# Kernel tuning notes

Measured on AMD Instinct MI355X. Metric: run time of the kernel, lower is better.

The kernel has to match this reference:

```python
import jax, jax.numpy as jnp
import numpy as np

BLOCK_SIZE = 64

def quantize_dequantize(w, block_size=BLOCK_SIZE):
    # LPBQ double quantization: block-wise abs-max -> uint4 scale1 over fp32 scale2
    out_ch, in_ch = w.shape
    pad_len = (block_size - in_ch % block_size) % block_size
    if pad_len > 0:
        w = jnp.pad(w, ((0, 0), (0, pad_len)))
    wr = w.reshape(out_ch, -1, block_size)                      # [O, nB, B]
    s1 = jnp.clip(jnp.max(jnp.abs(wr), axis=-1, keepdims=True) / 7.0, 1e-8)   # [O, nB, 1]
    s2 = jnp.clip(jnp.max(s1, axis=1, keepdims=True) / 15.0, 1e-8)            # [O, 1, 1]
    s1_q = jnp.clip(jnp.round(s1 / s2), 0.0, 15.0)
    s1_recon = s1_q * s2
    w_q = jnp.clip(jnp.round(wr / s1_recon), -8.0, 7.0)
    w_recon = (w_q * s1_recon).reshape(out_ch, -1)
    if pad_len > 0:
        w_recon = w_recon[:, :-pad_len]
    return w_recon

def setup_inputs() -> dict:
    key = jax.random.key(0)
    k1, k2, k3 = jax.random.split(key, 3)
    B, S, IN, OUT = 1, 128, 4096, 11008
    x = jax.random.normal(k1, (B, S, IN), dtype=jnp.float32)
    weight = jax.random.normal(k2, (OUT, IN), dtype=jnp.float32)
    bias = jax.random.normal(k3, (OUT,), dtype=jnp.float32)
    return {"x": x, "weight": weight, "bias": bias}

def reference(x, weight, bias):
    w_q = quantize_dequantize(weight)
    # F.linear: x @ w_q.T + bias
    return jnp.einsum('bsi,oi->bso', x, w_q) + bias
```

## Files before the change

kernel.cpp:

```cpp
#include <hip/hip_runtime.h>
#include <hip/hip_bf16.h>

#define IN_CH 4096
#define OUT_CH 11008
#define QBLK 64

#define BM 128
#define BN 64
#define BK 64
#define KCHUNKS (IN_CH / BK)
#define KSPLIT 4
#define SPLIT_CHUNKS (KCHUNKS / KSPLIT)
#define NTILES (OUT_CH / BN)
#define XCONV_BLOCKS 16
#define BPAD 72

typedef short bf16x8 __attribute__((ext_vector_type(8)));
typedef float f32x4 __attribute__((ext_vector_type(4)));

#define GLOBAL_AS __attribute__((address_space(1)))
#define LDS_AS __attribute__((address_space(3)))

__device__ inline unsigned short f2bf(float f) {
    union { __hip_bfloat16 h; unsigned short u; } cv;
    cv.h = __float2bfloat16(f);
    return cv.u;
}

__device__ inline void unpack8(unsigned v, float s1, bf16x8& o) {
#pragma unroll
    for (int i = 0; i < 4; ++i) {
        const int byte = (int)((v >> (8 * i)) & 0xFF);
        const int lo = (byte << 28) >> 28;
        const int hi = (byte << 24) >> 28;
        o[2 * i]     = (short)f2bf((float)lo * s1);
        o[2 * i + 1] = (short)f2bf((float)hi * s1);
    }
}

__global__ __launch_bounds__(256) void quant_kernel(
        const float* __restrict__ w, const float* __restrict__ x,
        signed char* __restrict__ wq, float* __restrict__ s1rT,
        unsigned short* __restrict__ xq) {
    const int tid = threadIdx.x;

    if (blockIdx.x >= OUT_CH) {
        const int bx = blockIdx.x - OUT_CH;
        for (int it = 0; it < 16; ++it) {
            const int G = it * 4096 + bx * 256 + tid;
            const int row = G >> 9;
            const int gi = G & 511;
            const int kc = gi >> 3;
            const int gp = gi & 7;
            const int gl = gp ^ (row & 7);
            const float4* src =
                (const float4*)(x + (size_t)row * IN_CH + kc * 64 + gl * 8);
            float4 a = src[0], b = src[1];
            ushort4 o0, o1;
            o0.x = f2bf(a.x); o0.y = f2bf(a.y); o0.z = f2bf(a.z); o0.w = f2bf(a.w);
            o1.x = f2bf(b.x); o1.y = f2bf(b.y); o1.z = f2bf(b.z); o1.w = f2bf(b.w);
            ushort4* dst = (ushort4*)(xq + (size_t)row * IN_CH + gi * 8);
            dst[0] = o0;
            dst[1] = o1;
        }
        return;
    }

    const int row = blockIdx.x;
    const float* wrow = w + (size_t)row * IN_CH;
    signed char* orow = wq + (size_t)row * (IN_CH / 2);

    __shared__ float s1_lds[64];

    float4 v[4];
    const int lane16 = tid & 15;

    for (int p = 0; p < 4; ++p) {
        v[p] = ((const float4*)wrow)[p * 256 + tid];
        float m = fmaxf(fmaxf(fabsf(v[p].x), fabsf(v[p].y)),
                        fmaxf(fabsf(v[p].z), fabsf(v[p].w)));
        m = fmaxf(m, __shfl_xor(m, 1));
        m = fmaxf(m, __shfl_xor(m, 2));
        m = fmaxf(m, __shfl_xor(m, 4));
        m = fmaxf(m, __shfl_xor(m, 8));
        if (lane16 == 0)
            s1_lds[p * 16 + (tid >> 4)] = fmaxf(m * (1.0f / 7.0f), 1e-8f);
    }
    __syncthreads();

    if (tid < 64) {
        float s1 = s1_lds[tid];
        float m = s1;
        m = fmaxf(m, __shfl_xor(m, 1));
        m = fmaxf(m, __shfl_xor(m, 2));
        m = fmaxf(m, __shfl_xor(m, 4));
        m = fmaxf(m, __shfl_xor(m, 8));
        m = fmaxf(m, __shfl_xor(m, 16));
        m = fmaxf(m, __shfl_xor(m, 32));
        const float s2 = fmaxf(m * (1.0f / 15.0f), 1e-8f);
        const float s1q = fminf(fmaxf(rintf(s1 / s2), 0.0f), 15.0f);
        const float s1r = s1q * s2;
        s1_lds[tid] = s1r;
        s1rT[(size_t)tid * OUT_CH + row] = s1r;
    }
    __syncthreads();

    for (int p = 0; p < 4; ++p) {
        const float s1r = s1_lds[p * 16 + (tid >> 4)];
        const int q0 = (int)fminf(fmaxf(rintf(v[p].x / s1r), -8.0f), 7.0f);
        const int q1 = (int)fminf(fmaxf(rintf(v[p].y / s1r), -8.0f), 7.0f);
        const int q2 = (int)fminf(fmaxf(rintf(v[p].z / s1r), -8.0f), 7.0f);
        const int q3 = (int)fminf(fmaxf(rintf(v[p].w / s1r), -8.0f), 7.0f);
        char2 o;
        o.x = (signed char)((q0 & 0xF) | ((q1 & 0xF) << 4));
        o.y = (signed char)((q2 & 0xF) | ((q3 & 0xF) << 4));
        ((char2*)orow)[p * 256 + tid] = o;
    }
}

__global__ __launch_bounds__(256) void gemm_kernel(
        const unsigned short* __restrict__ A, const signed char* __restrict__ WQ4,
        const float* __restrict__ s1rT, float* __restrict__ part) {
    __shared__ __align__(16) unsigned short ldsA[2][BM * BK];
    __shared__ __align__(16) unsigned short ldsB[2][BN * BPAD];

    const int tid = threadIdx.x;
    const int w = tid >> 6;
    const int l = tid & 63;
    const int wm = w >> 1;
    const int wn = w & 1;
    const int n0 = blockIdx.x * BN;
    const int kc0 = blockIdx.y * SPLIT_CHUNKS;

    const int r8 = l >> 3;
    const int sg = l & 7;

    const int brow = tid >> 2;
    const int bcg = tid & 3;

    const int lane15 = l & 15;
    const int quad = l >> 4;

    f32x4 acc[4][2] = {};

    const size_t bqBase = (size_t)(n0 + brow) * (IN_CH / 2) + bcg * 8;

    {
        const int k0 = kc0 * BK;
        for (int i = 0; i < 4; ++i) {
            const unsigned short* gp =
                A + (size_t)(i * 32 + w * 8 + r8) * IN_CH + k0 + sg * 8;
            LDS_AS unsigned short* lp =
                (LDS_AS unsigned short*)&ldsA[0][(i * 32 + w * 8) * BK];
            __builtin_amdgcn_global_load_lds((const GLOBAL_AS void*)gp,
                                             (LDS_AS void*)lp, 16, 0, 0);
        }
        const float s1 = s1rT[(size_t)kc0 * OUT_CH + n0 + brow];
        const uint2 bq = *(const uint2*)(WQ4 + bqBase + (size_t)kc0 * 32);
        bf16x8 o0, o1;
        unpack8(bq.x, s1, o0);
        unpack8(bq.y, s1, o1);
        *(bf16x8*)&ldsB[0][brow * BPAD + bcg * 16] = o0;
        *(bf16x8*)&ldsB[0][brow * BPAD + bcg * 16 + 8] = o1;
        asm volatile("s_waitcnt vmcnt(0)" ::: "memory");
        __syncthreads();
    }

    for (int t = 0; t < SPLIT_CHUNKS; ++t) {
        const int cur = t & 1;
        const int nxt = cur ^ 1;
        const bool has_next = (t + 1 < SPLIT_CHUNKS);

        uint2 bqn;
        float s1n;
        if (has_next) {
            const int kcn = kc0 + t + 1;
            const int k0n = kcn * BK;
            for (int i = 0; i < 4; ++i) {
                const unsigned short* gp =
                    A + (size_t)(i * 32 + w * 8 + r8) * IN_CH + k0n + sg * 8;
                LDS_AS unsigned short* lp =
                    (LDS_AS unsigned short*)&ldsA[nxt][(i * 32 + w * 8) * BK];
                __builtin_amdgcn_global_load_lds((const GLOBAL_AS void*)gp,
                                                 (LDS_AS void*)lp, 16, 0, 0);
            }
            s1n = s1rT[(size_t)kcn * OUT_CH + n0 + brow];
            bqn = *(const uint2*)(WQ4 + bqBase + (size_t)kcn * 32);
        }

        for (int kk = 0; kk < 2; ++kk) {
            bf16x8 af[4], bfv[2];
            const int ko = kk * 32 + quad * 8;
            for (int i = 0; i < 4; ++i) {
                const int row = wm * 64 + i * 16 + lane15;
                const int pg = ((kk * 4 + quad) ^ (row & 7)) * 8;
                af[i] = *(const bf16x8*)&ldsA[cur][row * BK + pg];
            }
            for (int j = 0; j < 2; ++j)
                bfv[j] = *(const bf16x8*)&ldsB[cur][(wn * 32 + j * 16 + lane15) * BPAD + ko];
            for (int i = 0; i < 4; ++i)
                for (int j = 0; j < 2; ++j)
                    acc[i][j] = __builtin_amdgcn_mfma_f32_16x16x32_bf16(
                        af[i], bfv[j], acc[i][j], 0, 0, 0);
        }

        if (has_next) {
            bf16x8 o0, o1;
            unpack8(bqn.x, s1n, o0);
            unpack8(bqn.y, s1n, o1);
            *(bf16x8*)&ldsB[nxt][brow * BPAD + bcg * 16] = o0;
            *(bf16x8*)&ldsB[nxt][brow * BPAD + bcg * 16 + 8] = o1;
            asm volatile("s_waitcnt vmcnt(0)" ::: "memory");
        }
        __syncthreads();
    }

    float* pbase = part + (size_t)blockIdx.y * BM * OUT_CH;
    const int m_base = wm * 64 + quad * 4;
    const int n_base = n0 + wn * 32 + lane15;
    for (int j = 0; j < 2; ++j) {
        for (int i = 0; i < 4; ++i) {
            const int m = m_base + i * 16;
            float* cp = pbase + (size_t)m * OUT_CH + n_base + j * 16;
            cp[0 * OUT_CH] = acc[i][j][0];
            cp[1 * OUT_CH] = acc[i][j][1];
            cp[2 * OUT_CH] = acc[i][j][2];
            cp[3 * OUT_CH] = acc[i][j][3];
        }
    }
}

__global__ __launch_bounds__(256) void reduce_kernel(
        const float* __restrict__ part, const float* __restrict__ bias,
        float* __restrict__ out) {
    const int m = blockIdx.y;
    const int x4 = blockIdx.x * 256 + threadIdx.x;
    if (x4 >= OUT_CH / 4) return;
    const size_t off = (size_t)m * OUT_CH + x4 * 4;

    float4 acc = ((const float4*)bias)[x4];
    for (int s = 0; s < KSPLIT; ++s) {
        float4 p = *(const float4*)(part + (size_t)s * BM * OUT_CH + off);
        acc.x += p.x; acc.y += p.y; acc.z += p.z; acc.w += p.w;
    }
    *(float4*)(out + off) = acc;
}

extern "C" void kernel_launch(void* const* d_in, const int* in_sizes, int n_in,
                              void* d_out, int out_size, void* d_ws, size_t ws_size,
                              hipStream_t stream) {
    const float* x = (const float*)d_in[0];
    const float* weight = (const float*)d_in[1];
    const float* bias = (const float*)d_in[2];
    float* out = (float*)d_out;

    signed char* wsQ = (signed char*)d_ws;
    unsigned short* wsX = (unsigned short*)(wsQ + (size_t)OUT_CH * (IN_CH / 2));
    float* wsS = (float*)(wsX + (size_t)BM * IN_CH);
    float* wsP = wsS + (size_t)QBLK * OUT_CH;

    quant_kernel<<<OUT_CH + XCONV_BLOCKS, 256, 0, stream>>>(weight, x, wsQ, wsS, wsX);
    gemm_kernel<<<dim3(NTILES, KSPLIT), 256, 0, stream>>>(wsX, wsQ, wsS, wsP);
    reduce_kernel<<<dim3((OUT_CH / 4 + 255) / 256, BM), 256, 0, stream>>>(
        wsP, bias, out);
}
```

Measured before the change: 293.8 us.

## Dequantize int4 weight fragments directly into MFMA registers, bypassing LDS

The GEMM no longer stages dequantized B tiles in shared memory. Each lane loads the packed int4 bytes for its own MFMA fragment and unpacks them straight into registers. Scales move to a row-major layout so each lane reads its row's scales contiguously. This removes the LDS writes and reads for B and halves LDS usage, which is also reflected in an occupancy hint. In exchange, waves sharing a column slice duplicate the dequantize work, and the 4-byte global loads are less coalesced.

```diff
diff --git a/kernel.cpp b/kernel.cpp
--- a/kernel.cpp
+++ b/kernel.cpp
@@ -13,7 +13,6 @@
 #define SPLIT_CHUNKS (KCHUNKS / KSPLIT)
 #define NTILES (OUT_CH / BN)
 #define XCONV_BLOCKS 16
-#define BPAD 72
 
 typedef short bf16x8 __attribute__((ext_vector_type(8)));
 typedef float f32x4 __attribute__((ext_vector_type(4)));
@@ -27,7 +26,8 @@
     return cv.u;
 }
 
-__device__ inline void unpack8(unsigned v, float s1, bf16x8& o) {
+__device__ inline bf16x8 unpack8(unsigned v, float s1) {
+    bf16x8 o;
 #pragma unroll
     for (int i = 0; i < 4; ++i) {
         const int byte = (int)((v >> (8 * i)) & 0xFF);
@@ -36,11 +36,12 @@
         o[2 * i]     = (short)f2bf((float)lo * s1);
         o[2 * i + 1] = (short)f2bf((float)hi * s1);
     }
+    return o;
 }
 
 __global__ __launch_bounds__(256) void quant_kernel(
         const float* __restrict__ w, const float* __restrict__ x,
-        signed char* __restrict__ wq, float* __restrict__ s1rT,
+        signed char* __restrict__ wq, float* __restrict__ s1rA,
         unsigned short* __restrict__ xq) {
     const int tid = threadIdx.x;
 
@@ -101,7 +102,7 @@
         const float s1q = fminf(fmaxf(rintf(s1 / s2), 0.0f), 15.0f);
         const float s1r = s1q * s2;
         s1_lds[tid] = s1r;
-        s1rT[(size_t)tid * OUT_CH + row] = s1r;
+        s1rA[(size_t)row * QBLK + tid] = s1r;
     }
     __syncthreads();
 
@@ -118,50 +119,53 @@
     }
 }
 
-__global__ __launch_bounds__(256) void gemm_kernel(
+__global__ __launch_bounds__(256, 4) void gemm_kernel(
         const unsigned short* __restrict__ A, const signed char* __restrict__ WQ4,
-        const float* __restrict__ s1rT, float* __restrict__ part) {
+        const float* __restrict__ s1rA, float* __restrict__ part) {
     __shared__ __align__(16) unsigned short ldsA[2][BM * BK];
-    __shared__ __align__(16) unsigned short ldsB[2][BN * BPAD];
 
     const int tid = threadIdx.x;
-    const int w = tid >> 6;
+    const int wid = tid >> 6;
     const int l = tid & 63;
-    const int wm = w >> 1;
-    const int wn = w & 1;
+    const int wm = wid >> 1;
+    const int wn = wid & 1;
     const int n0 = blockIdx.x * BN;
     const int kc0 = blockIdx.y * SPLIT_CHUNKS;
 
     const int r8 = l >> 3;
     const int sg = l & 7;
-
-    const int brow = tid >> 2;
-    const int bcg = tid & 3;
-
     const int lane15 = l & 15;
     const int quad = l >> 4;
 
     f32x4 acc[4][2] = {};
 
-    const size_t bqBase = (size_t)(n0 + brow) * (IN_CH / 2) + bcg * 8;
+    const int brow0 = n0 + wn * 32 + lane15;
+    const int brow1 = brow0 + 16;
+    const signed char* bq0 = WQ4 + (size_t)brow0 * (IN_CH / 2) + quad * 4;
+    const signed char* bq1 = WQ4 + (size_t)brow1 * (IN_CH / 2) + quad * 4;
+    const float* sp0 = s1rA + (size_t)brow0 * QBLK;
+    const float* sp1 = s1rA + (size_t)brow1 * QBLK;
+
+    unsigned cb00, cb01, cb10, cb11;
+    float cs0, cs1;
 
     {
+        const int boff = kc0 * 32;
+        cb00 = *(const unsigned*)(bq0 + boff);
+        cb01 = *(const unsigned*)(bq0 + boff + 16);
+        cb10 = *(const unsigned*)(bq1 + boff);
+        cb11 = *(const unsigned*)(bq1 + boff + 16);
+        cs0 = sp0[kc0];
+        cs1 = sp1[kc0];
         const int k0 = kc0 * BK;
         for (int i = 0; i < 4; ++i) {
             const unsigned short* gp =
-                A + (size_t)(i * 32 + w * 8 + r8) * IN_CH + k0 + sg * 8;
+                A + (size_t)(i * 32 + wid * 8 + r8) * IN_CH + k0 + sg * 8;
             LDS_AS unsigned short* lp =
-                (LDS_AS unsigned short*)&ldsA[0][(i * 32 + w * 8) * BK];
+                (LDS_AS unsigned short*)&ldsA[0][(i * 32 + wid * 8) * BK];
             __builtin_amdgcn_global_load_lds((const GLOBAL_AS void*)gp,
                                              (LDS_AS void*)lp, 16, 0, 0);
         }
-        const float s1 = s1rT[(size_t)kc0 * OUT_CH + n0 + brow];
-        const uint2 bq = *(const uint2*)(WQ4 + bqBase + (size_t)kc0 * 32);
-        bf16x8 o0, o1;
-        unpack8(bq.x, s1, o0);
-        unpack8(bq.y, s1, o1);
-        *(bf16x8*)&ldsB[0][brow * BPAD + bcg * 16] = o0;
-        *(bf16x8*)&ldsB[0][brow * BPAD + bcg * 16 + 8] = o1;
         asm volatile("s_waitcnt vmcnt(0)" ::: "memory");
         __syncthreads();
     }
@@ -171,45 +175,53 @@
         const int nxt = cur ^ 1;
         const bool has_next = (t + 1 < SPLIT_CHUNKS);
 
-        uint2 bqn;
-        float s1n;
+        unsigned nb00, nb01, nb10, nb11;
+        float ns0, ns1;
         if (has_next) {
             const int kcn = kc0 + t + 1;
+            const int boff = kcn * 32;
+            nb00 = *(const unsigned*)(bq0 + boff);
+            nb01 = *(const unsigned*)(bq0 + boff + 16);
+            nb10 = *(const unsigned*)(bq1 + boff);
+            nb11 = *(const unsigned*)(bq1 + boff + 16);
+            ns0 = sp0[kcn];
+            ns1 = sp1[kcn];
             const int k0n = kcn * BK;
             for (int i = 0; i < 4; ++i) {
                 const unsigned short* gp =
-                    A + (size_t)(i * 32 + w * 8 + r8) * IN_CH + k0n + sg * 8;
+                    A + (size_t)(i * 32 + wid * 8 + r8) * IN_CH + k0n + sg * 8;
                 LDS_AS unsigned short* lp =
-                    (LDS_AS unsigned short*)&ldsA[nxt][(i * 32 + w * 8) * BK];
+                    (LDS_AS unsigned short*)&ldsA[nxt][(i * 32 + wid * 8) * BK];
                 __builtin_amdgcn_global_load_lds((const GLOBAL_AS void*)gp,
                                                  (LDS_AS void*)lp, 16, 0, 0);
             }
-            s1n = s1rT[(size_t)kcn * OUT_CH + n0 + brow];
-            bqn = *(const uint2*)(WQ4 + bqBase + (size_t)kcn * 32);
-        }
+        }
+
+        bf16x8 bf00 = unpack8(cb00, cs0);
+        bf16x8 bf01 = unpack8(cb01, cs0);
+        bf16x8 bf10 = unpack8(cb10, cs1);
+        bf16x8 bf11 = unpack8(cb11, cs1);
 
         for (int kk = 0; kk < 2; ++kk) {
-            bf16x8 af[4], bfv[2];
-            const int ko = kk * 32 + quad * 8;
+            bf16x8 af[4];
             for (int i = 0; i < 4; ++i) {
                 const int row = wm * 64 + i * 16 + lane15;
                 const int pg = ((kk * 4 + quad) ^ (row & 7)) * 8;
                 af[i] = *(const bf16x8*)&ldsA[cur][row * BK + pg];
             }
-            for (int j = 0; j < 2; ++j)
-                bfv[j] = *(const bf16x8*)&ldsB[cur][(wn * 32 + j * 16 + lane15) * BPAD + ko];
-            for (int i = 0; i < 4; ++i)
-                for (int j = 0; j < 2; ++j)
-                    acc[i][j] = __builtin_amdgcn_mfma_f32_16x16x32_bf16(
-                        af[i], bfv[j], acc[i][j], 0, 0, 0);
+            const bf16x8 b0 = kk ? bf01 : bf00;
+            const bf16x8 b1 = kk ? bf11 : bf10;
+            for (int i = 0; i < 4; ++i) {
+                acc[i][0] = __builtin_amdgcn_mfma_f32_16x16x32_bf16(
+                    af[i], b0, acc[i][0], 0, 0, 0);
+                acc[i][1] = __builtin_amdgcn_mfma_f32_16x16x32_bf16(
+                    af[i], b1, acc[i][1], 0, 0, 0);
+            }
         }
 
         if (has_next) {
-            bf16x8 o0, o1;
-            unpack8(bqn.x, s1n, o0);
-            unpack8(bqn.y, s1n, o1);
-            *(bf16x8*)&ldsB[nxt][brow * BPAD + bcg * 16] = o0;
-            *(bf16x8*)&ldsB[nxt][brow * BPAD + bcg * 16 + 8] = o1;
+            cb00 = nb00; cb01 = nb01; cb10 = nb10; cb11 = nb11;
+            cs0 = ns0; cs1 = ns1;
             asm volatile("s_waitcnt vmcnt(0)" ::: "memory");
         }
         __syncthreads();
@@ -257,7 +269,7 @@
     signed char* wsQ = (signed char*)d_ws;
     unsigned short* wsX = (unsigned short*)(wsQ + (size_t)OUT_CH * (IN_CH / 2));
     float* wsS = (float*)(wsX + (size_t)BM * IN_CH);
-    float* wsP = wsS + (size_t)QBLK * OUT_CH;
+    float* wsP = wsS + (size_t)OUT_CH * QBLK;
 
     quant_kernel<<<OUT_CH + XCONV_BLOCKS, 256, 0, stream>>>(weight, x, wsQ, wsS, wsX);
     gemm_kernel<<<dim3(NTILES, KSPLIT), 256, 0, stream>>>(wsX, wsQ, wsS, wsP);
```

Result: slower. 309.0 us (+5.2%).

## Replace split-K partial buffer and reduce kernel with atomic accumulation into output

Applied to the files above, without the earlier changes.

Removes the separate reduce kernel and the KSPLIT partial-sum buffer. Output is pre-filled with bias by extra blocks in the quant kernel, and each split-K GEMM block adds its results with float atomics. The scale array is also transposed to a row-major [OUT][64] layout so GEMM scale loads come from one row. This cuts a kernel launch and about 22 MB of partial writes and reads, but adds atomic traffic and makes summation order nondeterministic.

```diff
diff --git a/kernel.cpp b/kernel.cpp
--- a/kernel.cpp
+++ b/kernel.cpp
@@ -13,6 +13,7 @@
 #define SPLIT_CHUNKS (KCHUNKS / KSPLIT)
 #define NTILES (OUT_CH / BN)
 #define XCONV_BLOCKS 16
+#define BIAS_BLOCKS 16
 #define BPAD 72
 
 typedef short bf16x8 __attribute__((ext_vector_type(8)));
@@ -40,9 +41,20 @@
 
 __global__ __launch_bounds__(256) void quant_kernel(
         const float* __restrict__ w, const float* __restrict__ x,
-        signed char* __restrict__ wq, float* __restrict__ s1rT,
-        unsigned short* __restrict__ xq) {
+        const float* __restrict__ bias, signed char* __restrict__ wq,
+        float* __restrict__ s1rA, unsigned short* __restrict__ xq,
+        float* __restrict__ out) {
     const int tid = threadIdx.x;
+
+    if (blockIdx.x >= OUT_CH + XCONV_BLOCKS) {
+        const int bx = blockIdx.x - OUT_CH - XCONV_BLOCKS;
+        const float4* b4 = (const float4*)bias;
+        float4* o4 = (float4*)out;
+        for (int q = bx * 256 + tid; q < BM * OUT_CH / 4;
+             q += BIAS_BLOCKS * 256)
+            o4[q] = b4[q % (OUT_CH / 4)];
+        return;
+    }
 
     if (blockIdx.x >= OUT_CH) {
         const int bx = blockIdx.x - OUT_CH;
@@ -101,7 +113,7 @@
         const float s1q = fminf(fmaxf(rintf(s1 / s2), 0.0f), 15.0f);
         const float s1r = s1q * s2;
         s1_lds[tid] = s1r;
-        s1rT[(size_t)tid * OUT_CH + row] = s1r;
+        s1rA[(size_t)row * QBLK + tid] = s1r;
     }
     __syncthreads();
 
@@ -120,7 +132,7 @@
 
 __global__ __launch_bounds__(256) void gemm_kernel(
         const unsigned short* __restrict__ A, const signed char* __restrict__ WQ4,
-        const float* __restrict__ s1rT, float* __restrict__ part) {
+        const float* __restrict__ s1rA, float* __restrict__ out) {
     __shared__ __align__(16) unsigned short ldsA[2][BM * BK];
     __shared__ __align__(16) unsigned short ldsB[2][BN * BPAD];
 
@@ -144,6 +156,7 @@
     f32x4 acc[4][2] = {};
 
     const size_t bqBase = (size_t)(n0 + brow) * (IN_CH / 2) + bcg * 8;
+    const float* sRow = s1rA + (size_t)(n0 + brow) * QBLK;
 
     {
         const int k0 = kc0 * BK;
@@ -155,7 +168,7 @@
             __builtin_amdgcn_global_load_lds((const GLOBAL_AS void*)gp,
                                              (LDS_AS void*)lp, 16, 0, 0);
         }
-        const float s1 = s1rT[(size_t)kc0 * OUT_CH + n0 + brow];
+        const float s1 = sRow[kc0];
         const uint2 bq = *(const uint2*)(WQ4 + bqBase + (size_t)kc0 * 32);
         bf16x8 o0, o1;
         unpack8(bq.x, s1, o0);
@@ -184,7 +197,7 @@
                 __builtin_amdgcn_global_load_lds((const GLOBAL_AS void*)gp,
                                                  (LDS_AS void*)lp, 16, 0, 0);
             }
-            s1n = s1rT[(size_t)kcn * OUT_CH + n0 + brow];
+            s1n = sRow[kcn];
             bqn = *(const uint2*)(WQ4 + bqBase + (size_t)kcn * 32);
         }
 
@@ -215,35 +228,18 @@
         __syncthreads();
     }
 
-    float* pbase = part + (size_t)blockIdx.y * BM * OUT_CH;
     const int m_base = wm * 64 + quad * 4;
     const int n_base = n0 + wn * 32 + lane15;
     for (int j = 0; j < 2; ++j) {
         for (int i = 0; i < 4; ++i) {
             const int m = m_base + i * 16;
-            float* cp = pbase + (size_t)m * OUT_CH + n_base + j * 16;
-            cp[0 * OUT_CH] = acc[i][j][0];
-            cp[1 * OUT_CH] = acc[i][j][1];
-            cp[2 * OUT_CH] = acc[i][j][2];
-            cp[3 * OUT_CH] = acc[i][j][3];
-        }
-    }
-}
-
-__global__ __launch_bounds__(256) void reduce_kernel(
-        const float* __restrict__ part, const float* __restrict__ bias,
-        float* __restrict__ out) {
-    const int m = blockIdx.y;
-    const int x4 = blockIdx.x * 256 + threadIdx.x;
-    if (x4 >= OUT_CH / 4) return;
-    const size_t off = (size_t)m * OUT_CH + x4 * 4;
-
-    float4 acc = ((const float4*)bias)[x4];
-    for (int s = 0; s < KSPLIT; ++s) {
-        float4 p = *(const float4*)(part + (size_t)s * BM * OUT_CH + off);
-        acc.x += p.x; acc.y += p.y; acc.z += p.z; acc.w += p.w;
-    }
-    *(float4*)(out + off) = acc;
+            float* cp = out + (size_t)m * OUT_CH + n_base + j * 16;
+            unsafeAtomicAdd(cp + 0 * OUT_CH, acc[i][j][0]);
+            unsafeAtomicAdd(cp + 1 * OUT_CH, acc[i][j][1]);
+            unsafeAtomicAdd(cp + 2 * OUT_CH, acc[i][j][2]);
+            unsafeAtomicAdd(cp + 3 * OUT_CH, acc[i][j][3]);
+        }
+    }
 }
 
 extern "C" void kernel_launch(void* const* d_in, const int* in_sizes, int n_in,
@@ -257,10 +253,8 @@
     signed char* wsQ = (signed char*)d_ws;
     unsigned short* wsX = (unsigned short*)(wsQ + (size_t)OUT_CH * (IN_CH / 2));
     float* wsS = (float*)(wsX + (size_t)BM * IN_CH);
-    float* wsP = wsS + (size_t)QBLK * OUT_CH;
-
-    quant_kernel<<<OUT_CH + XCONV_BLOCKS, 256, 0, stream>>>(weight, x, wsQ, wsS, wsX);
-    gemm_kernel<<<dim3(NTILES, KSPLIT), 256, 0, stream>>>(wsX, wsQ, wsS, wsP);
-    reduce_kernel<<<dim3((OUT_CH / 4 + 255) / 256, BM), 256, 0, stream>>>(
-        wsP, bias, out);
-}
+
+    quant_kernel<<<OUT_CH + XCONV_BLOCKS + BIAS_BLOCKS, 256, 0, stream>>>(
+        weight, x, bias, wsQ, wsS, wsX, out);
+    gemm_kernel<<<dim3(NTILES, KSPLIT), 256, 0, stream>>>(wsX, wsQ, wsS, out);
+}
```

New measurement: 303.7 us. +3.4%, slower.
